# Optimization experiments

Hardware: AMD Instinct MI355X
Metric: run time of the kernel (lower is better)

Reference implementation:

```python
import jax, jax.numpy as jnp
import numpy as np

D_MODEL = 768
M_DIM = 256
N_HEADS = 4
B, N = 16, 4096


def _l2norm(v):
    # F.normalize(dim=-1): v / max(||v||, 1e-12)
    return v / jnp.maximum(jnp.linalg.norm(v, axis=-1, keepdims=True), 1e-12)


def setup_inputs() -> dict:
    key = jax.random.key(0)
    ks = jax.random.split(key, 16)
    x = jax.random.normal(ks[0], (B, N, D_MODEL), dtype=jnp.float32)
    # frozen random projections (std 1.0 / 0.5 / 0.1), torch Linear weight layout [out, in]
    Wr1 = jax.random.normal(ks[1], (M_DIM, D_MODEL), dtype=jnp.float32) * 1.0
    Wr2 = jax.random.normal(ks[2], (M_DIM, D_MODEL), dtype=jnp.float32) * 0.5
    Wr3 = jax.random.normal(ks[3], (M_DIM, D_MODEL), dtype=jnp.float32) * 0.1
    # learned projection + LayerNorm
    Wl = jax.random.normal(ks[4], (M_DIM, D_MODEL), dtype=jnp.float32) * 0.02
    bl = jnp.zeros((M_DIM,), jnp.float32)
    ln_g = jnp.ones((M_DIM,), jnp.float32)
    ln_b = jnp.zeros((M_DIM,), jnp.float32)
    # MultiheadAttention in-proj (q,k,v) and out-proj
    Wq = jax.random.normal(ks[5], (M_DIM, M_DIM), dtype=jnp.float32) * 0.02
    Wk = jax.random.normal(ks[6], (M_DIM, M_DIM), dtype=jnp.float32) * 0.02
    Wv = jax.random.normal(ks[7], (M_DIM, M_DIM), dtype=jnp.float32) * 0.02
    bq = jnp.zeros((M_DIM,), jnp.float32)
    bk = jnp.zeros((M_DIM,), jnp.float32)
    bv = jnp.zeros((M_DIM,), jnp.float32)
    Wo = jax.random.normal(ks[8], (M_DIM, M_DIM), dtype=jnp.float32) * 0.02
    bo = jnp.zeros((M_DIM,), jnp.float32)
    return {"x": x, "Wr1": Wr1, "Wr2": Wr2, "Wr3": Wr3, "Wl": Wl, "bl": bl,
            "ln_g": ln_g, "ln_b": ln_b, "Wq": Wq, "bq": bq, "Wk": Wk, "bk": bk,
            "Wv": Wv, "bv": bv, "Wo": Wo, "bo": bo}


def reference(x, Wr1, Wr2, Wr3, Wl, bl, ln_g, ln_b, Wq, bq, Wk, bk, Wv, bv, Wo, bo):
    Bx, Nx, D = x.shape
    T = Bx * Nx
    xf = x.reshape(T, D)
    # three frozen random-projection branches, each L2-normalized
    r1 = _l2norm(xf @ Wr1.T)
    r2 = _l2norm(xf @ Wr2.T)
    r3 = _l2norm(xf @ Wr3.T)
    # learned branch: Linear -> LayerNorm (dropout is identity in eval) -> normalize
    h = xf @ Wl.T + bl
    mu = jnp.mean(h, axis=-1, keepdims=True)
    var = jnp.var(h, axis=-1, keepdims=True)
    h = (h - mu) / jnp.sqrt(var + 1e-5) * ln_g + ln_b
    lf = _l2norm(h)
    feats = jnp.stack([r1, r2, r3, lf], axis=1)  # [T, 4, M]
    q = jnp.mean(feats, axis=1, keepdims=True)   # [T, 1, M]
    M = feats.shape[-1]
    hd = M // N_HEADS
    qh = (q @ Wq.T + bq).reshape(T, 1, N_HEADS, hd)
    kh = (feats @ Wk.T + bk).reshape(T, 4, N_HEADS, hd)
    vh = (feats @ Wv.T + bv).reshape(T, 4, N_HEADS, hd)
    scores = jnp.einsum('tqhd,tkhd->thqk', qh, kh) / jnp.sqrt(jnp.float32(hd))
    attn = jax.nn.softmax(scores, axis=-1)       # softmax over the 4 branches
    fused = jnp.einsum('thqk,tkhd->tqhd', attn, vh).reshape(T, M)
    out = fused @ Wo.T + bo
    return _l2norm(out).reshape(Bx, Nx, M)
```

## Files before the change

kernel.cpp:

```cpp
#include <hip/hip_runtime.h>
#include <stdint.h>

#define TOK 65536
#define DMODEL 768

typedef short  s16x8 __attribute__((ext_vector_type(8)));
typedef __bf16 bf16x8 __attribute__((ext_vector_type(8)));
typedef float  f32x4 __attribute__((ext_vector_type(4)));

__device__ __forceinline__ float b2f(unsigned short u) {
  union { unsigned int i; float f; } v; v.i = ((unsigned int)u) << 16; return v.f;
}
__device__ __forceinline__ unsigned short f2b(float f) {
  union { float f; unsigned int i; } v; v.f = f;
  unsigned int r = v.i + 0x7fffu + ((v.i >> 16) & 1u);
  return (unsigned short)(r >> 16);
}
__device__ __forceinline__ float wsum(float v) {
#pragma unroll
  for (int off = 32; off >= 1; off >>= 1) v += __shfl_xor(v, off, 64);
  return v;
}

template <bool BF16_OUT, bool HAS_BIAS>
__global__ void gemm_bt(const unsigned short* __restrict__ A,
                        const unsigned short* __restrict__ W,
                        void* __restrict__ Cv,
                        const float* __restrict__ bias,
                        int M, int N, int K, int nt) {
  __shared__ __align__(16) unsigned short As[128 * 64];
  __shared__ __align__(16) unsigned short Bs[128 * 64];
  const int tid  = threadIdx.x;
  const int lane = tid & 63;
  const int w    = tid >> 6;
  const int wr   = w >> 1, wc = w & 1;
  const int l16  = lane & 15, lh = lane >> 4;

  const int per = gridDim.x >> 3;
  const int bid = blockIdx.x;
  const int wg  = (bid & 7) * per + (bid >> 3);
  const long arow0 = (long)(wg / nt) * 128;
  const long bcol0 = (long)(wg % nt) * 128;

  f32x4 acc[4][4];
#pragma unroll
  for (int mi = 0; mi < 4; ++mi)
#pragma unroll
    for (int ni = 0; ni < 4; ++ni) acc[mi][ni] = f32x4{0.f, 0.f, 0.f, 0.f};

  const int srow = lane >> 3;
  const int scol = ((lane & 7) ^ (srow & 7)) * 8;

  for (int k0 = 0; k0 < K; k0 += 64) {
#pragma unroll
    for (int i = 0; i < 4; ++i) {
      int sec = i * 4 + w;
      int row = sec * 8 + srow;
      const unsigned short* ga = A + (arow0 + row) * (long)K + k0 + scol;
      const unsigned short* gb = W + (bcol0 + row) * (long)K + k0 + scol;
      __builtin_amdgcn_global_load_lds(
          (const __attribute__((address_space(1))) void*)ga,
          (__attribute__((address_space(3))) void*)&As[sec * 512], 16, 0, 0);
      __builtin_amdgcn_global_load_lds(
          (const __attribute__((address_space(1))) void*)gb,
          (__attribute__((address_space(3))) void*)&Bs[sec * 512], 16, 0, 0);
    }
    __syncthreads();
#pragma unroll
    for (int kk = 0; kk < 2; ++kk) {
      bf16x8 af[4], bf[4];
      const int sw = (l16 & 7) << 3;
#pragma unroll
      for (int mi = 0; mi < 4; ++mi)
        af[mi] = __builtin_bit_cast(bf16x8,
            *(const s16x8*)&As[(((wr * 64 + mi * 16 + l16) * 64) + kk * 32 + lh * 8) ^ sw]);
#pragma unroll
      for (int ni = 0; ni < 4; ++ni)
        bf[ni] = __builtin_bit_cast(bf16x8,
            *(const s16x8*)&Bs[(((wc * 64 + ni * 16 + l16) * 64) + kk * 32 + lh * 8) ^ sw]);
#pragma unroll
      for (int mi = 0; mi < 4; ++mi)
#pragma unroll
        for (int ni = 0; ni < 4; ++ni)
          acc[mi][ni] = __builtin_amdgcn_mfma_f32_16x16x32_bf16(af[mi], bf[ni], acc[mi][ni], 0, 0, 0);
    }
    __syncthreads();
  }

#pragma unroll
  for (int mi = 0; mi < 4; ++mi)
#pragma unroll
    for (int ni = 0; ni < 4; ++ni)
#pragma unroll
      for (int j = 0; j < 4; ++j) {
        long row = arow0 + wr * 64 + mi * 16 + lh * 4 + j;
        long col = bcol0 + wc * 64 + ni * 16 + l16;
        float v = acc[mi][ni][j];
        if (HAS_BIAS) v += bias[col];
        if (BF16_OUT) ((unsigned short*)Cv)[row * N + col] = f2b(v);
        else          ((float*)Cv)[row * N + col] = v;
      }
}

__global__ void cast_x_kernel(const float* __restrict__ x, unsigned short* __restrict__ xb) {
  long i = ((long)blockIdx.x * 256 + threadIdx.x) * 4;
  float4 v = *reinterpret_cast<const float4*>(x + i);
  ushort4 o = {f2b(v.x), f2b(v.y), f2b(v.z), f2b(v.w)};
  *reinterpret_cast<ushort4*>(xb + i) = o;
}

__global__ void prep_wall_kernel(const float* __restrict__ Wr1, const float* __restrict__ Wr2,
                                 const float* __restrict__ Wr3, const float* __restrict__ Wl,
                                 unsigned short* __restrict__ Wall) {
  int idx = blockIdx.x * 256 + threadIdx.x;
  int base = idx * 4;
  int n = base / DMODEL, k = base % DMODEL;
  const float* src = (n < 256)  ? Wr1 + (long)n * DMODEL
                   : (n < 512)  ? Wr2 + (long)(n - 256) * DMODEL
                   : (n < 768)  ? Wr3 + (long)(n - 512) * DMODEL
                                : Wl  + (long)(n - 768) * DMODEL;
  float4 v = *reinterpret_cast<const float4*>(src + k);
  ushort4 o = {f2b(v.x), f2b(v.y), f2b(v.z), f2b(v.w)};
  *reinterpret_cast<ushort4*>(Wall + base) = o;
}

__global__ void prep_G_kernel(const float* __restrict__ Wq, const float* __restrict__ Wk,
                              const float* __restrict__ bq, unsigned short* __restrict__ Wg,
                              float* __restrict__ dvec) {
  int idx = blockIdx.x * 256 + threadIdx.x;
  int n = idx >> 8, a = idx & 255;
  int h = n >> 8, b = n & 255;
  const float* wq = Wq + (long)(h * 64) * 256 + a;
  const float* wk = Wk + (long)(h * 64) * 256 + b;
  float s = 0.f;
  for (int d = 0; d < 64; ++d) s += wq[d * 256] * wk[d * 256];
  Wg[(long)n * 256 + a] = f2b(s);
  if (a == 0) {
    float t = 0.f;
    const float* bqh = bq + h * 64;
    for (int d = 0; d < 64; ++d) t += bqh[d] * wk[d * 256];
    dvec[n] = t;
  }
}

__global__ void prep_P_kernel(const float* __restrict__ Wo, const float* __restrict__ Wv,
                              const float* __restrict__ bv, const float* __restrict__ bo,
                              unsigned short* __restrict__ Wp, float* __restrict__ bo2) {
  int idx = blockIdx.x * 256 + threadIdx.x;
  int m = idx >> 10, n = idx & 1023;
  int h = n >> 8, b = n & 255;
  const float* wo = Wo + (long)m * 256 + h * 64;
  const float* wv = Wv + (long)(h * 64) * 256 + b;
  float s = 0.f;
  for (int d = 0; d < 64; ++d) s += wo[d] * wv[d * 256];
  Wp[(long)m * 1024 + n] = f2b(s);
  if (n == 0) {
    float t = bo[m];
    const float* wor = Wo + (long)m * 256;
    for (int j = 0; j < 256; ++j) t += wor[j] * bv[j];
    bo2[m] = t;
  }
}

__global__ void norm_kernel(unsigned short* __restrict__ H, unsigned short* __restrict__ q,
                            const float* __restrict__ bl, const float* __restrict__ lng,
                            const float* __restrict__ lnb) {
  int token = blockIdx.x * 4 + (threadIdx.x >> 6);
  int lane = threadIdx.x & 63;
  unsigned short* row = H + (long)token * 1024;
  int b0 = lane * 4;
  float h[4][4];
#pragma unroll
  for (int s = 0; s < 4; ++s) {
    ushort4 v = *reinterpret_cast<const ushort4*>(row + s * 256 + b0);
    h[s][0] = b2f(v.x); h[s][1] = b2f(v.y); h[s][2] = b2f(v.z); h[s][3] = b2f(v.w);
  }
  float4 blv = *reinterpret_cast<const float4*>(bl + b0);
  h[3][0] += blv.x; h[3][1] += blv.y; h[3][2] += blv.z; h[3][3] += blv.w;

  float ss0 = 0, ss1 = 0, ss2 = 0, s3 = 0, ss3 = 0;
#pragma unroll
  for (int j = 0; j < 4; ++j) {
    ss0 += h[0][j] * h[0][j];
    ss1 += h[1][j] * h[1][j];
    ss2 += h[2][j] * h[2][j];
    s3  += h[3][j];
    ss3 += h[3][j] * h[3][j];
  }
  ss0 = wsum(ss0); ss1 = wsum(ss1); ss2 = wsum(ss2); s3 = wsum(s3); ss3 = wsum(ss3);
  float i0 = 1.f / fmaxf(sqrtf(ss0), 1e-12f);
  float i1 = 1.f / fmaxf(sqrtf(ss1), 1e-12f);
  float i2 = 1.f / fmaxf(sqrtf(ss2), 1e-12f);
  float mu = s3 * (1.f / 256.f);
  float var = ss3 * (1.f / 256.f) - mu * mu;
  float is = rsqrtf(var + 1e-5f);
  float4 gv = *reinterpret_cast<const float4*>(lng + b0);
  float4 bv = *reinterpret_cast<const float4*>(lnb + b0);
  float hn[4];
  hn[0] = (h[3][0] - mu) * is * gv.x + bv.x;
  hn[1] = (h[3][1] - mu) * is * gv.y + bv.y;
  hn[2] = (h[3][2] - mu) * is * gv.z + bv.z;
  hn[3] = (h[3][3] - mu) * is * gv.w + bv.w;
  float ssn = hn[0]*hn[0] + hn[1]*hn[1] + hn[2]*hn[2] + hn[3]*hn[3];
  ssn = wsum(ssn);
  float i3 = 1.f / fmaxf(sqrtf(ssn), 1e-12f);

  float f0[4], f1[4], f2[4], f3[4], qv[4];
#pragma unroll
  for (int j = 0; j < 4; ++j) {
    f0[j] = h[0][j] * i0; f1[j] = h[1][j] * i1; f2[j] = h[2][j] * i2; f3[j] = hn[j] * i3;
    qv[j] = 0.25f * (f0[j] + f1[j] + f2[j] + f3[j]);
  }
  ushort4 o0 = {f2b(f0[0]), f2b(f0[1]), f2b(f0[2]), f2b(f0[3])};
  ushort4 o1 = {f2b(f1[0]), f2b(f1[1]), f2b(f1[2]), f2b(f1[3])};
  ushort4 o2 = {f2b(f2[0]), f2b(f2[1]), f2b(f2[2]), f2b(f2[3])};
  ushort4 o3 = {f2b(f3[0]), f2b(f3[1]), f2b(f3[2]), f2b(f3[3])};
  ushort4 oq = {f2b(qv[0]), f2b(qv[1]), f2b(qv[2]), f2b(qv[3])};
  *reinterpret_cast<ushort4*>(row + 0 * 256 + b0) = o0;
  *reinterpret_cast<ushort4*>(row + 1 * 256 + b0) = o1;
  *reinterpret_cast<ushort4*>(row + 2 * 256 + b0) = o2;
  *reinterpret_cast<ushort4*>(row + 3 * 256 + b0) = o3;
  *reinterpret_cast<ushort4*>(q + (long)token * 256 + b0) = oq;
}

__global__ void attn_kernel(unsigned short* __restrict__ U, const unsigned short* __restrict__ F) {
  int token = blockIdx.x * 4 + (threadIdx.x >> 6);
  int lane = threadIdx.x & 63;
  unsigned short* urow = U + (long)token * 1024;
  const unsigned short* frow = F + (long)token * 1024;
  int b0 = lane * 4;
  float u[4][4], f[4][4];
#pragma unroll
  for (int s = 0; s < 4; ++s) {
    ushort4 uv = *reinterpret_cast<const ushort4*>(urow + s * 256 + b0);
    ushort4 fv = *reinterpret_cast<const ushort4*>(frow + s * 256 + b0);
    u[s][0] = b2f(uv.x); u[s][1] = b2f(uv.y); u[s][2] = b2f(uv.z); u[s][3] = b2f(uv.w);
    f[s][0] = b2f(fv.x); f[s][1] = b2f(fv.y); f[s][2] = b2f(fv.z); f[s][3] = b2f(fv.w);
  }
  float sc[4][4];
#pragma unroll
  for (int h = 0; h < 4; ++h)
#pragma unroll
    for (int k = 0; k < 4; ++k) {
      float s = 0.f;
#pragma unroll
      for (int j = 0; j < 4; ++j) s += u[h][j] * f[k][j];
      sc[h][k] = wsum(s);
    }
  float g[4][4];
#pragma unroll
  for (int h = 0; h < 4; ++h) {
    float m = fmaxf(fmaxf(sc[h][0], sc[h][1]), fmaxf(sc[h][2], sc[h][3]));
    float e0 = __expf((sc[h][0] - m) * 0.125f);
    float e1 = __expf((sc[h][1] - m) * 0.125f);
    float e2 = __expf((sc[h][2] - m) * 0.125f);
    float e3 = __expf((sc[h][3] - m) * 0.125f);
    float inv = 1.f / (e0 + e1 + e2 + e3);
#pragma unroll
    for (int j = 0; j < 4; ++j)
      g[h][j] = (e0 * f[0][j] + e1 * f[1][j] + e2 * f[2][j] + e3 * f[3][j]) * inv;
  }
#pragma unroll
  for (int h = 0; h < 4; ++h) {
    ushort4 o = {f2b(g[h][0]), f2b(g[h][1]), f2b(g[h][2]), f2b(g[h][3])};
    *reinterpret_cast<ushort4*>(urow + h * 256 + b0) = o;
  }
}

__global__ void l2_out_kernel(const float* __restrict__ in, float* __restrict__ out) {
  int token = blockIdx.x * 4 + (threadIdx.x >> 6);
  int lane = threadIdx.x & 63;
  float4 v = reinterpret_cast<const float4*>(in + (long)token * 256)[lane];
  float ss = wsum(v.x * v.x + v.y * v.y + v.z * v.z + v.w * v.w);
  float inv = 1.f / fmaxf(sqrtf(ss), 1e-12f);
  float4 o = {v.x * inv, v.y * inv, v.z * inv, v.w * inv};
  reinterpret_cast<float4*>(out + (long)token * 256)[lane] = o;
}

extern "C" void kernel_launch(void* const* d_in, const int* in_sizes, int n_in,
                              void* d_out, int out_size, void* d_ws, size_t ws_size,
                              hipStream_t stream) {
  const float* x   = (const float*)d_in[0];
  const float* Wr1 = (const float*)d_in[1];
  const float* Wr2 = (const float*)d_in[2];
  const float* Wr3 = (const float*)d_in[3];
  const float* Wl  = (const float*)d_in[4];
  const float* bl  = (const float*)d_in[5];
  const float* lng = (const float*)d_in[6];
  const float* lnb = (const float*)d_in[7];
  const float* Wq  = (const float*)d_in[8];
  const float* bq  = (const float*)d_in[9];
  const float* Wk  = (const float*)d_in[10];
  const float* Wv  = (const float*)d_in[12];
  const float* bv  = (const float*)d_in[13];
  const float* Wo  = (const float*)d_in[14];
  const float* bo  = (const float*)d_in[15];

  char* ws = (char*)d_ws;
  size_t off = 0;
  auto alloc = [&](size_t bytes) -> void* {
    void* p = ws + off;
    off += (bytes + 255) & ~(size_t)255;
    return p;
  };
  unsigned short* xbf  = (unsigned short*)alloc((size_t)TOK * DMODEL * 2);
  unsigned short* H    = (unsigned short*)alloc((size_t)TOK * 1024 * 2);
  unsigned short* qb   = (unsigned short*)alloc((size_t)TOK * 256 * 2);
  unsigned short* U    = (unsigned short*)alloc((size_t)TOK * 1024 * 2);
  unsigned short* Wall = (unsigned short*)alloc((size_t)1024 * DMODEL * 2);
  unsigned short* Wg   = (unsigned short*)alloc((size_t)1024 * 256 * 2);
  unsigned short* Wp   = (unsigned short*)alloc((size_t)256 * 1024 * 2);
  float* dvec = (float*)alloc(1024 * 4);
  float* bo2  = (float*)alloc(256 * 4);
  float* outpre = (float*)xbf;

  cast_x_kernel<<<(TOK * DMODEL) / 1024, 256, 0, stream>>>(x, xbf);
  prep_wall_kernel<<<(1024 * DMODEL) / 1024, 256, 0, stream>>>(Wr1, Wr2, Wr3, Wl, Wall);
  prep_G_kernel<<<1024, 256, 0, stream>>>(Wq, Wk, bq, Wg, dvec);
  prep_P_kernel<<<1024, 256, 0, stream>>>(Wo, Wv, bv, bo, Wp, bo2);

  gemm_bt<true, false><<<4096, 256, 0, stream>>>(xbf, Wall, H, nullptr, TOK, 1024, DMODEL, 8);
  norm_kernel<<<TOK / 4, 256, 0, stream>>>(H, qb, bl, lng, lnb);
  gemm_bt<true, true><<<4096, 256, 0, stream>>>(qb, Wg, U, dvec, TOK, 1024, 256, 8);
  attn_kernel<<<TOK / 4, 256, 0, stream>>>(U, H);
  gemm_bt<false, true><<<1024, 256, 0, stream>>>(U, Wp, outpre, bo2, TOK, 256, 1024, 2);
  l2_out_kernel<<<TOK / 4, 256, 0, stream>>>(outpre, (float*)d_out);

  (void)in_sizes; (void)n_in; (void)out_size; (void)ws_size;
}
```

Baseline: 728.9 us.

## Fuse x cast into first GEMM, double-buffer GEMMs, fuse output L2 norm

The first GEMM now reads fp32 x directly, converts it to bf16 in registers and writes it to LDS, so the separate cast kernel and its bf16 copy of x are gone. All GEMMs get double-buffered LDS so the next K tile loads while the current one computes. The last GEMM becomes a 128x256 full-row tile kernel that adds the bias and applies the final L2 normalization in its epilogue, removing the fp32 intermediate and the separate l2_out kernel. The norm and attention kernels switch to 32 lanes per token with 8-wide vector loads and stores. In exchange, LDS use grows and register pressure rises from the fp32 A staging.

```diff
diff --git a/kernel.cpp b/kernel.cpp
--- a/kernel.cpp
+++ b/kernel.cpp
@@ -16,20 +16,20 @@
   unsigned int r = v.i + 0x7fffu + ((v.i >> 16) & 1u);
   return (unsigned short)(r >> 16);
 }
-__device__ __forceinline__ float wsum(float v) {
-#pragma unroll
-  for (int off = 32; off >= 1; off >>= 1) v += __shfl_xor(v, off, 64);
+__device__ __forceinline__ float wsum32(float v) {
+#pragma unroll
+  for (int off = 16; off >= 1; off >>= 1) v += __shfl_xor(v, off, 64);
   return v;
 }
 
-template <bool BF16_OUT, bool HAS_BIAS>
-__global__ void gemm_bt(const unsigned short* __restrict__ A,
+template <bool BF16_OUT, bool HAS_BIAS, bool A_F32>
+__global__ __launch_bounds__(256) void gemm_bt(const void* __restrict__ Av,
                         const unsigned short* __restrict__ W,
                         void* __restrict__ Cv,
                         const float* __restrict__ bias,
                         int M, int N, int K, int nt) {
-  __shared__ __align__(16) unsigned short As[128 * 64];
-  __shared__ __align__(16) unsigned short Bs[128 * 64];
+  __shared__ __align__(16) unsigned short As[2][128 * 64];
+  __shared__ __align__(16) unsigned short Bs[2][128 * 64];
   const int tid  = threadIdx.x;
   const int lane = tid & 63;
   const int w    = tid >> 6;
@@ -42,30 +42,67 @@
   const long arow0 = (long)(wg / nt) * 128;
   const long bcol0 = (long)(wg % nt) * 128;
 
+  const int srow = lane >> 3;
+  const int scol = ((lane & 7) ^ srow) * 8;
+
+  const int ar  = tid >> 1;
+  const int ac0 = (tid & 1) * 4;
+
+  const unsigned short* Au = (const unsigned short*)Av;
+  const float* Af = (const float*)Av;
+
   f32x4 acc[4][4];
 #pragma unroll
   for (int mi = 0; mi < 4; ++mi)
 #pragma unroll
     for (int ni = 0; ni < 4; ++ni) acc[mi][ni] = f32x4{0.f, 0.f, 0.f, 0.f};
 
-  const int srow = lane >> 3;
-  const int scol = ((lane & 7) ^ (srow & 7)) * 8;
-
-  for (int k0 = 0; k0 < K; k0 += 64) {
+  float4 areg[8];
+
+  auto stage_b = [&](int b, int k0) {
 #pragma unroll
     for (int i = 0; i < 4; ++i) {
       int sec = i * 4 + w;
       int row = sec * 8 + srow;
-      const unsigned short* ga = A + (arow0 + row) * (long)K + k0 + scol;
       const unsigned short* gb = W + (bcol0 + row) * (long)K + k0 + scol;
       __builtin_amdgcn_global_load_lds(
+          (const __attribute__((address_space(1))) void*)gb,
+          (__attribute__((address_space(3))) void*)&Bs[b][sec * 512], 16, 0, 0);
+    }
+  };
+  auto stage_a_lds = [&](int b, int k0) {
+#pragma unroll
+    for (int i = 0; i < 4; ++i) {
+      int sec = i * 4 + w;
+      int row = sec * 8 + srow;
+      const unsigned short* ga = Au + (arow0 + row) * (long)K + k0 + scol;
+      __builtin_amdgcn_global_load_lds(
           (const __attribute__((address_space(1))) void*)ga,
-          (__attribute__((address_space(3))) void*)&As[sec * 512], 16, 0, 0);
-      __builtin_amdgcn_global_load_lds(
-          (const __attribute__((address_space(1))) void*)gb,
-          (__attribute__((address_space(3))) void*)&Bs[sec * 512], 16, 0, 0);
-    }
-    __syncthreads();
+          (__attribute__((address_space(3))) void*)&As[b][sec * 512], 16, 0, 0);
+    }
+  };
+  auto load_a_f32 = [&](int k0) {
+#pragma unroll
+    for (int q = 0; q < 4; ++q) {
+      const float* p = Af + (arow0 + ar) * (long)K + k0 + (ac0 + q) * 8;
+      areg[2 * q]     = *reinterpret_cast<const float4*>(p);
+      areg[2 * q + 1] = *reinterpret_cast<const float4*>(p + 4);
+    }
+  };
+  auto write_a = [&](int b) {
+#pragma unroll
+    for (int q = 0; q < 4; ++q) {
+      float4 v0 = areg[2 * q], v1 = areg[2 * q + 1];
+      s16x8 o;
+      o[0] = (short)f2b(v0.x); o[1] = (short)f2b(v0.y);
+      o[2] = (short)f2b(v0.z); o[3] = (short)f2b(v0.w);
+      o[4] = (short)f2b(v1.x); o[5] = (short)f2b(v1.y);
+      o[6] = (short)f2b(v1.z); o[7] = (short)f2b(v1.w);
+      int dst = ar * 64 + (((ac0 + q) ^ (ar & 7)) * 8);
+      *(s16x8*)&As[b][dst] = o;
+    }
+  };
+  auto compute = [&](int b) {
 #pragma unroll
     for (int kk = 0; kk < 2; ++kk) {
       bf16x8 af[4], bf[4];
@@ -73,18 +110,36 @@
 #pragma unroll
       for (int mi = 0; mi < 4; ++mi)
         af[mi] = __builtin_bit_cast(bf16x8,
-            *(const s16x8*)&As[(((wr * 64 + mi * 16 + l16) * 64) + kk * 32 + lh * 8) ^ sw]);
+            *(const s16x8*)&As[b][(((wr * 64 + mi * 16 + l16) * 64) + kk * 32 + lh * 8) ^ sw]);
 #pragma unroll
       for (int ni = 0; ni < 4; ++ni)
         bf[ni] = __builtin_bit_cast(bf16x8,
-            *(const s16x8*)&Bs[(((wc * 64 + ni * 16 + l16) * 64) + kk * 32 + lh * 8) ^ sw]);
+            *(const s16x8*)&Bs[b][(((wc * 64 + ni * 16 + l16) * 64) + kk * 32 + lh * 8) ^ sw]);
 #pragma unroll
       for (int mi = 0; mi < 4; ++mi)
 #pragma unroll
         for (int ni = 0; ni < 4; ++ni)
           acc[mi][ni] = __builtin_amdgcn_mfma_f32_16x16x32_bf16(af[mi], bf[ni], acc[mi][ni], 0, 0, 0);
     }
+  };
+
+  const int nsteps = K >> 6;
+  if (A_F32) { load_a_f32(0); stage_b(0, 0); write_a(0); }
+  else       { stage_a_lds(0, 0); stage_b(0, 0); }
+  __syncthreads();
+  int cur = 0;
+  for (int s = 0; s < nsteps; ++s) {
+    int nxt = cur ^ 1;
+    bool has = (s + 1 < nsteps);
+    if (has) {
+      if (A_F32) load_a_f32((s + 1) << 6);
+      else       stage_a_lds(nxt, (s + 1) << 6);
+      stage_b(nxt, (s + 1) << 6);
+    }
+    compute(cur);
+    if (A_F32 && has) write_a(nxt);
     __syncthreads();
+    cur = nxt;
   }
 
 #pragma unroll
@@ -102,11 +157,115 @@
       }
 }
 
-__global__ void cast_x_kernel(const float* __restrict__ x, unsigned short* __restrict__ xb) {
-  long i = ((long)blockIdx.x * 256 + threadIdx.x) * 4;
-  float4 v = *reinterpret_cast<const float4*>(x + i);
-  ushort4 o = {f2b(v.x), f2b(v.y), f2b(v.z), f2b(v.w)};
-  *reinterpret_cast<ushort4*>(xb + i) = o;
+__global__ __launch_bounds__(512) void gemm3_fused(
+    const unsigned short* __restrict__ G, const unsigned short* __restrict__ Wp,
+    const float* __restrict__ bo2, float* __restrict__ out) {
+  __shared__ __align__(16) unsigned short As[2][128 * 64];
+  __shared__ __align__(16) unsigned short Bs[2][256 * 64];
+  __shared__ float ss[128][4];
+  const int tid  = threadIdx.x;
+  const int lane = tid & 63;
+  const int w    = tid >> 6;
+  const int wr   = w >> 2, wc = w & 3;
+  const int l16  = lane & 15, lh = lane >> 4;
+  const int per  = gridDim.x >> 3;
+  const int bid  = blockIdx.x;
+  const int wg   = (bid & 7) * per + (bid >> 3);
+  const long arow0 = (long)wg * 128;
+  const int srow = lane >> 3;
+  const int scol = ((lane & 7) ^ srow) * 8;
+
+  f32x4 acc[4][4];
+#pragma unroll
+  for (int mi = 0; mi < 4; ++mi)
+#pragma unroll
+    for (int ni = 0; ni < 4; ++ni) acc[mi][ni] = f32x4{0.f, 0.f, 0.f, 0.f};
+
+  auto stage = [&](int b, int k0) {
+#pragma unroll
+    for (int i = 0; i < 2; ++i) {
+      int sec = i * 8 + w;
+      int row = sec * 8 + srow;
+      const unsigned short* ga = G + (arow0 + row) * 1024L + k0 + scol;
+      __builtin_amdgcn_global_load_lds(
+          (const __attribute__((address_space(1))) void*)ga,
+          (__attribute__((address_space(3))) void*)&As[b][sec * 512], 16, 0, 0);
+    }
+#pragma unroll
+    for (int i = 0; i < 4; ++i) {
+      int sec = i * 8 + w;
+      int row = sec * 8 + srow;
+      const unsigned short* gb = Wp + (long)row * 1024 + k0 + scol;
+      __builtin_amdgcn_global_load_lds(
+          (const __attribute__((address_space(1))) void*)gb,
+          (__attribute__((address_space(3))) void*)&Bs[b][sec * 512], 16, 0, 0);
+    }
+  };
+  auto compute = [&](int b) {
+#pragma unroll
+    for (int kk = 0; kk < 2; ++kk) {
+      bf16x8 af[4], bf[4];
+      const int sw = (l16 & 7) << 3;
+#pragma unroll
+      for (int mi = 0; mi < 4; ++mi)
+        af[mi] = __builtin_bit_cast(bf16x8,
+            *(const s16x8*)&As[b][(((wr * 64 + mi * 16 + l16) * 64) + kk * 32 + lh * 8) ^ sw]);
+#pragma unroll
+      for (int ni = 0; ni < 4; ++ni)
+        bf[ni] = __builtin_bit_cast(bf16x8,
+            *(const s16x8*)&Bs[b][(((wc * 64 + ni * 16 + l16) * 64) + kk * 32 + lh * 8) ^ sw]);
+#pragma unroll
+      for (int mi = 0; mi < 4; ++mi)
+#pragma unroll
+        for (int ni = 0; ni < 4; ++ni)
+          acc[mi][ni] = __builtin_amdgcn_mfma_f32_16x16x32_bf16(af[mi], bf[ni], acc[mi][ni], 0, 0, 0);
+    }
+  };
+
+  stage(0, 0);
+  __syncthreads();
+  int cur = 0;
+  for (int s = 0; s < 16; ++s) {
+    int nxt = cur ^ 1;
+    if (s + 1 < 16) stage(nxt, (s + 1) << 6);
+    compute(cur);
+    __syncthreads();
+    cur = nxt;
+  }
+
+  float bo2v[4];
+#pragma unroll
+  for (int ni = 0; ni < 4; ++ni) bo2v[ni] = bo2[wc * 64 + ni * 16 + l16];
+#pragma unroll
+  for (int mi = 0; mi < 4; ++mi)
+#pragma unroll
+    for (int ni = 0; ni < 4; ++ni)
+#pragma unroll
+      for (int j = 0; j < 4; ++j) acc[mi][ni][j] += bo2v[ni];
+#pragma unroll
+  for (int mi = 0; mi < 4; ++mi)
+#pragma unroll
+    for (int j = 0; j < 4; ++j) {
+      float p = 0.f;
+#pragma unroll
+      for (int ni = 0; ni < 4; ++ni) p += acc[mi][ni][j] * acc[mi][ni][j];
+#pragma unroll
+      for (int off = 8; off >= 1; off >>= 1) p += __shfl_xor(p, off, 64);
+      if (l16 == 0) ss[wr * 64 + mi * 16 + lh * 4 + j][wc] = p;
+    }
+  __syncthreads();
+#pragma unroll
+  for (int mi = 0; mi < 4; ++mi)
+#pragma unroll
+    for (int j = 0; j < 4; ++j) {
+      int r = wr * 64 + mi * 16 + lh * 4 + j;
+      float tot = ss[r][0] + ss[r][1] + ss[r][2] + ss[r][3];
+      float inv = 1.f / fmaxf(sqrtf(tot), 1e-12f);
+      long row = arow0 + r;
+#pragma unroll
+      for (int ni = 0; ni < 4; ++ni)
+        out[row * 256 + wc * 64 + ni * 16 + l16] = acc[mi][ni][j] * inv;
+    }
 }
 
 __global__ void prep_wall_kernel(const float* __restrict__ Wr1, const float* __restrict__ Wr2,
@@ -165,77 +324,86 @@
 __global__ void norm_kernel(unsigned short* __restrict__ H, unsigned short* __restrict__ q,
                             const float* __restrict__ bl, const float* __restrict__ lng,
                             const float* __restrict__ lnb) {
-  int token = blockIdx.x * 4 + (threadIdx.x >> 6);
-  int lane = threadIdx.x & 63;
+  int token = blockIdx.x * 8 + (threadIdx.x >> 5);
+  int l = threadIdx.x & 31;
   unsigned short* row = H + (long)token * 1024;
-  int b0 = lane * 4;
-  float h[4][4];
+  int b0 = l * 8;
+  float h[4][8];
 #pragma unroll
   for (int s = 0; s < 4; ++s) {
-    ushort4 v = *reinterpret_cast<const ushort4*>(row + s * 256 + b0);
-    h[s][0] = b2f(v.x); h[s][1] = b2f(v.y); h[s][2] = b2f(v.z); h[s][3] = b2f(v.w);
-  }
-  float4 blv = *reinterpret_cast<const float4*>(bl + b0);
-  h[3][0] += blv.x; h[3][1] += blv.y; h[3][2] += blv.z; h[3][3] += blv.w;
+    s16x8 v = *(const s16x8*)(row + s * 256 + b0);
+#pragma unroll
+    for (int j = 0; j < 8; ++j) h[s][j] = b2f((unsigned short)v[j]);
+  }
+  float blv[8];
+  *(float4*)&blv[0] = *(const float4*)(bl + b0);
+  *(float4*)&blv[4] = *(const float4*)(bl + b0 + 4);
+#pragma unroll
+  for (int j = 0; j < 8; ++j) h[3][j] += blv[j];
 
   float ss0 = 0, ss1 = 0, ss2 = 0, s3 = 0, ss3 = 0;
 #pragma unroll
-  for (int j = 0; j < 4; ++j) {
+  for (int j = 0; j < 8; ++j) {
     ss0 += h[0][j] * h[0][j];
     ss1 += h[1][j] * h[1][j];
     ss2 += h[2][j] * h[2][j];
     s3  += h[3][j];
     ss3 += h[3][j] * h[3][j];
   }
-  ss0 = wsum(ss0); ss1 = wsum(ss1); ss2 = wsum(ss2); s3 = wsum(s3); ss3 = wsum(ss3);
+  ss0 = wsum32(ss0); ss1 = wsum32(ss1); ss2 = wsum32(ss2);
+  s3 = wsum32(s3); ss3 = wsum32(ss3);
   float i0 = 1.f / fmaxf(sqrtf(ss0), 1e-12f);
   float i1 = 1.f / fmaxf(sqrtf(ss1), 1e-12f);
   float i2 = 1.f / fmaxf(sqrtf(ss2), 1e-12f);
   float mu = s3 * (1.f / 256.f);
   float var = ss3 * (1.f / 256.f) - mu * mu;
-  float is = rsqrtf(var + 1e-5f);
-  float4 gv = *reinterpret_cast<const float4*>(lng + b0);
-  float4 bv = *reinterpret_cast<const float4*>(lnb + b0);
-  float hn[4];
-  hn[0] = (h[3][0] - mu) * is * gv.x + bv.x;
-  hn[1] = (h[3][1] - mu) * is * gv.y + bv.y;
-  hn[2] = (h[3][2] - mu) * is * gv.z + bv.z;
-  hn[3] = (h[3][3] - mu) * is * gv.w + bv.w;
-  float ssn = hn[0]*hn[0] + hn[1]*hn[1] + hn[2]*hn[2] + hn[3]*hn[3];
-  ssn = wsum(ssn);
+  float isd = rsqrtf(var + 1e-5f);
+  float gv[8], bvv[8];
+  *(float4*)&gv[0] = *(const float4*)(lng + b0);
+  *(float4*)&gv[4] = *(const float4*)(lng + b0 + 4);
+  *(float4*)&bvv[0] = *(const float4*)(lnb + b0);
+  *(float4*)&bvv[4] = *(const float4*)(lnb + b0 + 4);
+  float hn[8];
+  float ssn = 0.f;
+#pragma unroll
+  for (int j = 0; j < 8; ++j) {
+    hn[j] = (h[3][j] - mu) * isd * gv[j] + bvv[j];
+    ssn += hn[j] * hn[j];
+  }
+  ssn = wsum32(ssn);
   float i3 = 1.f / fmaxf(sqrtf(ssn), 1e-12f);
 
-  float f0[4], f1[4], f2[4], f3[4], qv[4];
-#pragma unroll
-  for (int j = 0; j < 4; ++j) {
-    f0[j] = h[0][j] * i0; f1[j] = h[1][j] * i1; f2[j] = h[2][j] * i2; f3[j] = hn[j] * i3;
-    qv[j] = 0.25f * (f0[j] + f1[j] + f2[j] + f3[j]);
-  }
-  ushort4 o0 = {f2b(f0[0]), f2b(f0[1]), f2b(f0[2]), f2b(f0[3])};
-  ushort4 o1 = {f2b(f1[0]), f2b(f1[1]), f2b(f1[2]), f2b(f1[3])};
-  ushort4 o2 = {f2b(f2[0]), f2b(f2[1]), f2b(f2[2]), f2b(f2[3])};
-  ushort4 o3 = {f2b(f3[0]), f2b(f3[1]), f2b(f3[2]), f2b(f3[3])};
-  ushort4 oq = {f2b(qv[0]), f2b(qv[1]), f2b(qv[2]), f2b(qv[3])};
-  *reinterpret_cast<ushort4*>(row + 0 * 256 + b0) = o0;
-  *reinterpret_cast<ushort4*>(row + 1 * 256 + b0) = o1;
-  *reinterpret_cast<ushort4*>(row + 2 * 256 + b0) = o2;
-  *reinterpret_cast<ushort4*>(row + 3 * 256 + b0) = o3;
-  *reinterpret_cast<ushort4*>(q + (long)token * 256 + b0) = oq;
+  s16x8 o0, o1, o2, o3, oq;
+#pragma unroll
+  for (int j = 0; j < 8; ++j) {
+    float f0 = h[0][j] * i0, f1 = h[1][j] * i1, f2 = h[2][j] * i2, f3 = hn[j] * i3;
+    o0[j] = (short)f2b(f0); o1[j] = (short)f2b(f1);
+    o2[j] = (short)f2b(f2); o3[j] = (short)f2b(f3);
+    oq[j] = (short)f2b(0.25f * (f0 + f1 + f2 + f3));
+  }
+  *(s16x8*)(row + 0 * 256 + b0) = o0;
+  *(s16x8*)(row + 1 * 256 + b0) = o1;
+  *(s16x8*)(row + 2 * 256 + b0) = o2;
+  *(s16x8*)(row + 3 * 256 + b0) = o3;
+  *(s16x8*)(q + (long)token * 256 + b0) = oq;
 }
 
 __global__ void attn_kernel(unsigned short* __restrict__ U, const unsigned short* __restrict__ F) {
-  int token = blockIdx.x * 4 + (threadIdx.x >> 6);
-  int lane = threadIdx.x & 63;
+  int token = blockIdx.x * 8 + (threadIdx.x >> 5);
+  int l = threadIdx.x & 31;
   unsigned short* urow = U + (long)token * 1024;
   const unsigned short* frow = F + (long)token * 1024;
-  int b0 = lane * 4;
-  float u[4][4], f[4][4];
+  int b0 = l * 8;
+  float u[4][8], f[4][8];
 #pragma unroll
   for (int s = 0; s < 4; ++s) {
-    ushort4 uv = *reinterpret_cast<const ushort4*>(urow + s * 256 + b0);
-    ushort4 fv = *reinterpret_cast<const ushort4*>(frow + s * 256 + b0);
-    u[s][0] = b2f(uv.x); u[s][1] = b2f(uv.y); u[s][2] = b2f(uv.z); u[s][3] = b2f(uv.w);
-    f[s][0] = b2f(fv.x); f[s][1] = b2f(fv.y); f[s][2] = b2f(fv.z); f[s][3] = b2f(fv.w);
+    s16x8 uv = *(const s16x8*)(urow + s * 256 + b0);
+    s16x8 fv = *(const s16x8*)(frow + s * 256 + b0);
+#pragma unroll
+    for (int j = 0; j < 8; ++j) {
+      u[s][j] = b2f((unsigned short)uv[j]);
+      f[s][j] = b2f((unsigned short)fv[j]);
+    }
   }
   float sc[4][4];
 #pragma unroll
@@ -244,10 +412,9 @@
     for (int k = 0; k < 4; ++k) {
       float s = 0.f;
 #pragma unroll
-      for (int j = 0; j < 4; ++j) s += u[h][j] * f[k][j];
-      sc[h][k] = wsum(s);
-    }
-  float g[4][4];
+      for (int j = 0; j < 8; ++j) s += u[h][j] * f[k][j];
+      sc[h][k] = wsum32(s);
+    }
 #pragma unroll
   for (int h = 0; h < 4; ++h) {
     float m = fmaxf(fmaxf(sc[h][0], sc[h][1]), fmaxf(sc[h][2], sc[h][3]));
@@ -256,25 +423,12 @@
     float e2 = __expf((sc[h][2] - m) * 0.125f);
     float e3 = __expf((sc[h][3] - m) * 0.125f);
     float inv = 1.f / (e0 + e1 + e2 + e3);
-#pragma unroll
-    for (int j = 0; j < 4; ++j)
-      g[h][j] = (e0 * f[0][j] + e1 * f[1][j] + e2 * f[2][j] + e3 * f[3][j]) * inv;
-  }
-#pragma unroll
-  for (int h = 0; h < 4; ++h) {
-    ushort4 o = {f2b(g[h][0]), f2b(g[h][1]), f2b(g[h][2]), f2b(g[h][3])};
-    *reinterpret_cast<ushort4*>(urow + h * 256 + b0) = o;
-  }
-}
-
-__global__ void l2_out_kernel(const float* __restrict__ in, float* __restrict__ out) {
-  int token = blockIdx.x * 4 + (threadIdx.x >> 6);
-  int lane = threadIdx.x & 63;
-  float4 v = reinterpret_cast<const float4*>(in + (long)token * 256)[lane];
-  float ss = wsum(v.x * v.x + v.y * v.y + v.z * v.z + v.w * v.w);
-  float inv = 1.f / fmaxf(sqrtf(ss), 1e-12f);
-  float4 o = {v.x * inv, v.y * inv, v.z * inv, v.w * inv};
-  reinterpret_cast<float4*>(out + (long)token * 256)[lane] = o;
+    s16x8 o;
+#pragma unroll
+    for (int j = 0; j < 8; ++j)
+      o[j] = (short)f2b((e0 * f[0][j] + e1 * f[1][j] + e2 * f[2][j] + e3 * f[3][j]) * inv);
+    *(s16x8*)(urow + h * 256 + b0) = o;
+  }
 }
 
 extern "C" void kernel_launch(void* const* d_in, const int* in_sizes, int n_in,
@@ -303,7 +457,6 @@
     off += (bytes + 255) & ~(size_t)255;
     return p;
   };
-  unsigned short* xbf  = (unsigned short*)alloc((size_t)TOK * DMODEL * 2);
   unsigned short* H    = (unsigned short*)alloc((size_t)TOK * 1024 * 2);
   unsigned short* qb   = (unsigned short*)alloc((size_t)TOK * 256 * 2);
   unsigned short* U    = (unsigned short*)alloc((size_t)TOK * 1024 * 2);
@@ -312,19 +465,16 @@
   unsigned short* Wp   = (unsigned short*)alloc((size_t)256 * 1024 * 2);
   float* dvec = (float*)alloc(1024 * 4);
   float* bo2  = (float*)alloc(256 * 4);
-  float* outpre = (float*)xbf;
-
-  cast_x_kernel<<<(TOK * DMODEL) / 1024, 256, 0, stream>>>(x, xbf);
+
   prep_wall_kernel<<<(1024 * DMODEL) / 1024, 256, 0, stream>>>(Wr1, Wr2, Wr3, Wl, Wall);
   prep_G_kernel<<<1024, 256, 0, stream>>>(Wq, Wk, bq, Wg, dvec);
   prep_P_kernel<<<1024, 256, 0, stream>>>(Wo, Wv, bv, bo, Wp, bo2);
 
-  gemm_bt<true, false><<<4096, 256, 0, stream>>>(xbf, Wall, H, nullptr, TOK, 1024, DMODEL, 8);
-  norm_kernel<<<TOK / 4, 256, 0, stream>>>(H, qb, bl, lng, lnb);
-  gemm_bt<true, true><<<4096, 256, 0, stream>>>(qb, Wg, U, dvec, TOK, 1024, 256, 8);
-  attn_kernel<<<TOK / 4, 256, 0, stream>>>(U, H);
-  gemm_bt<false, true><<<1024, 256, 0, stream>>>(U, Wp, outpre, bo2, TOK, 256, 1024, 2);
-  l2_out_kernel<<<TOK / 4, 256, 0, stream>>>(outpre, (float*)d_out);
+  gemm_bt<true, false, true><<<4096, 256, 0, stream>>>((const void*)x, Wall, H, nullptr, TOK, 1024, DMODEL, 8);
+  norm_kernel<<<TOK / 8, 256, 0, stream>>>(H, qb, bl, lng, lnb);
+  gemm_bt<true, true, false><<<4096, 256, 0, stream>>>((const void*)qb, Wg, U, dvec, TOK, 1024, 256, 8);
+  attn_kernel<<<TOK / 8, 256, 0, stream>>>(U, H);
+  gemm3_fused<<<512, 512, 0, stream>>>(U, Wp, bo2, (float*)d_out);
 
   (void)in_sizes; (void)n_in; (void)out_size; (void)ws_size;
 }
```

Measured after the change: 823.1 us. 1.13x slower.
